# Kernel tuning notes

Hardware: AMD Instinct MI355X
Metric: run time of the kernel (lower is better)

## Reference

```python
import jax, jax.numpy as jnp
import numpy as np

# TT structure: W is [in_features, out_features] = [4096, 4096]
IN_FACTORS = (16, 16, 16)
OUT_FACTORS = (16, 16, 16)
RANKS = (1, 8, 8, 1)
BATCH = 8192
IN_FEATURES = 4096
OUT_FEATURES = 4096
ITER_NUM = 3
L = 1.0
S = -1.0
EPSILON = 1.0


def tt_dense_matmul(cores, mat):
    """Multiply TT-matrix (cores[k]: [r_{k-1}, m_k, n_k, r_k]) by dense mat [prod(n), P].
    Returns [prod(m), P]. Sequential core contractions, never materializes dense W."""
    P = mat.shape[1]
    data = mat.reshape(1, mat.shape[0], P)  # [r=1, N_rem, T]
    M = 1
    for core in cores:
        r0, m, n, r1 = core.shape
        nrem = data.shape[1]
        d4 = data.reshape(r0, n, nrem // n, -1)            # [r0, n_k, N_rem', T]
        data = jnp.einsum('rmns,rnat->satm', core, d4)      # [r1, N_rem', T, m_k]
        data = data.reshape(r1, nrem // n, -1)              # fold m_k into trailing T
        M *= m
    return data.reshape(P, M).T  # [M, P]


def tt_tt_mul(cores_a, cores_b):
    """TT-matrix product: cores of A [M,K] and B [K,N] -> cores of A@B with Kronecker ranks."""
    out = []
    for ca, cb in zip(cores_a, cores_b):
        a0, m, n, a1 = ca.shape
        b0, n2, l, b1 = cb.shape
        c = jnp.einsum('amnb,cnld->acmlbd', ca, cb)
        out.append(c.reshape(a0 * b0, m, l, a1 * b1))
    return out


def setup_inputs() -> dict:
    key = jax.random.key(0)
    ks = jax.random.split(key, 5)
    x = jax.random.normal(ks[0], (BATCH, IN_FEATURES), dtype=jnp.float32)
    # TT cores of weight W [in, out]: core_k shape [r_{k-1}, in_k, out_k, r_k]
    core_std = 0.3  # glorot-like per-core scale
    cores = []
    for k in range(3):
        shp = (RANKS[k], IN_FACTORS[k], OUT_FACTORS[k], RANKS[k + 1])
        cores.append(core_std * jax.random.normal(ks[k + 1], shp, dtype=jnp.float32))
    bias = 0.01 * jnp.ones((OUT_FEATURES,), dtype=jnp.float32)
    return {"x": x, "core0": cores[0], "core1": cores[1], "core2": cores[2], "bias": bias}


def reference(x, core0, core1, core2, bias):
    cores = [core0, core1, core2]
    # weight_t = t3.transpose(weight): swap in/out mode of each core
    cores_t = [c.transpose(0, 2, 1, 3) for c in cores]  # W^T: [out, in]
    x_t = x.T  # [in, B]
    mv = tt_dense_matmul(cores_t, x_t).T  # x @ W, [B, out]
    # norm-gated shrinkage init
    norm_x = jnp.linalg.norm(x)
    x_l = (mv + bias) / L + jnp.where(norm_x > EPSILON, 0.0, S)
    # G = W^T @ W in TT form (ranks grow to 64)
    G = tt_tt_mul(cores_t, cores)
    for _ in range(1, ITER_NUM):
        nrm = jnp.linalg.norm(x_l)
        term = tt_dense_matmul(G, x_l.T).T  # x_l @ (W^T W), [B, out]
        x_l = x_l - term / L + mv / L + bias + jnp.where(nrm > EPSILON, 0.0, S)
    return x_l
```

## Files before the change

### kernel.cpp

```cpp
#include <hip/hip_runtime.h>
#include <stdint.h>

typedef __bf16 bf16;
typedef __bf16 bf16x4 __attribute__((ext_vector_type(4)));
typedef __bf16 bf16x8 __attribute__((ext_vector_type(8)));
typedef float f32x4 __attribute__((ext_vector_type(4)));

#define GLD_LDS16(g, l)                                                        \
  __builtin_amdgcn_global_load_lds(                                            \
      (const __attribute__((address_space(1))) void*)(g),                      \
      (__attribute__((address_space(3))) void*)(l), 16, 0, 0)

#define BAR() asm volatile("s_barrier" ::: "memory")
#define LGKM0() asm volatile("s_waitcnt lgkmcnt(0)" ::: "memory")
#define VMW(n) asm volatile("s_waitcnt vmcnt(" #n ")" ::: "memory")
#define PRIO(x) __builtin_amdgcn_s_setprio(x)

__global__ void k_init(float* s) {
  if (threadIdx.x < 3) s[threadIdx.x] = 0.0f;
}

__global__ void k_cast_ssq(const float* __restrict__ x, bf16* __restrict__ xb,
                           float* __restrict__ ssq, int n4) {
  int tid = blockIdx.x * blockDim.x + threadIdx.x;
  int stride = gridDim.x * blockDim.x;
  const float4* x4 = (const float4*)x;
  bf16x4* xb4 = (bf16x4*)xb;
  float acc = 0.f;
  for (int i = tid; i < n4; i += stride) {
    float4 v = x4[i];
    acc += v.x * v.x + v.y * v.y + v.z * v.z + v.w * v.w;
    bf16x4 b;
    b.x = (bf16)v.x; b.y = (bf16)v.y; b.z = (bf16)v.z; b.w = (bf16)v.w;
    xb4[i] = b;
  }
#pragma unroll
  for (int off = 32; off; off >>= 1) acc += __shfl_down(acc, off);
  __shared__ float red[4];
  if ((threadIdx.x & 63) == 0) red[threadIdx.x >> 6] = acc;
  __syncthreads();
  if (threadIdx.x == 0) atomicAdd(ssq, red[0] + red[1] + red[2] + red[3]);
}

__global__ void k_buildW(const float* __restrict__ c0, const float* __restrict__ c1,
                         const float* __restrict__ c2, bf16* __restrict__ Wt) {
  int t = blockIdx.x * 256 + threadIdx.x;
  int j = t >> 8;
  int i0 = (t >> 4) & 15;
  int i1 = t & 15;
  int j0 = j >> 8, j1 = (j >> 4) & 15, j2 = j & 15;
  float t0[8];
#pragma unroll
  for (int r1 = 0; r1 < 8; ++r1) t0[r1] = c0[(i0 * 16 + j0) * 8 + r1];
  float a[8];
#pragma unroll
  for (int r2 = 0; r2 < 8; ++r2) {
    float s = 0.f;
#pragma unroll
    for (int r1 = 0; r1 < 8; ++r1) s += t0[r1] * c1[((r1 * 16 + i1) * 16 + j1) * 8 + r2];
    a[r2] = s;
  }
  union { bf16 h[16]; bf16x8 v[2]; } u;
#pragma unroll
  for (int i2 = 0; i2 < 16; ++i2) {
    float s = 0.f;
#pragma unroll
    for (int r2 = 0; r2 < 8; ++r2) s += a[r2] * c2[(r2 * 16 + i2) * 16 + j2];
    u.h[i2] = (bf16)s;
  }
  bf16* dst = Wt + (size_t)j * 4096 + i0 * 256 + i1 * 16;
  ((bf16x8*)dst)[0] = u.v[0];
  ((bf16x8*)dst)[1] = u.v[1];
}

template <int MODE>
__global__ __launch_bounds__(512, 2) void k_gemm(
    const bf16* __restrict__ A, const bf16* __restrict__ Bt, int M, int N, int K,
    const float* __restrict__ bias, const bf16* __restrict__ xl0,
    const bf16* __restrict__ xl_prev, float* f32_out, bf16* __restrict__ bf_out,
    const float* __restrict__ ssq_a, const float* __restrict__ ssq_b,
    float* __restrict__ ssq_out) {
  const int nb = gridDim.x * gridDim.y;
  const int lin = blockIdx.y * gridDim.x + blockIdx.x;
  const int sw = (lin & 7) * (nb >> 3) + (lin >> 3);
  const int bx = sw % gridDim.x, by = sw / gridDim.x;
  if constexpr (MODE == 1) {
    if (bx < by) return;
  }

  __shared__ char smem[131072];

  const int t = threadIdx.x;
  const int w = t >> 6, lane = t & 63;
  const int q = lane >> 4, lr = lane & 15;
  const int wm = w & 1, wn = w >> 1;

  float gate = 0.f;
  if constexpr (MODE == 0) {
    gate = (*ssq_a > 1.0f) ? 0.f : -1.f;
  } else if constexpr (MODE == 2 || MODE == 3) {
    float g0 = (*ssq_a > 1.0f) ? 0.f : -1.f;
    float gt = (*ssq_b > 1.0f) ? 0.f : -1.f;
    gate = gt - g0;
  }
  VMW(0);

  const int r0 = t >> 3;
  const int ksrc = (t & 7) ^ (r0 & 7);
  const bf16* srcA = A + (size_t)(by * 256 + r0) * K + ksrc * 8;
  const bf16* srcB = Bt + (size_t)(bx * 256 + r0) * K + ksrc * 8;
  const int wofs = w << 10;

#define STAGE_A(h, kt, b)                                                              \
  do {                                                                                 \
    GLD_LDS16(srcA + (size_t)((h) * 128) * K + (kt) * 64,                              \
              smem + (b) * 65536 + (h) * 16384 + wofs);                                \
    GLD_LDS16(srcA + (size_t)((h) * 128 + 64) * K + (kt) * 64,                         \
              smem + (b) * 65536 + (h) * 16384 + 8192 + wofs);                         \
  } while (0)
#define STAGE_B(h, kt, b)                                                              \
  do {                                                                                 \
    GLD_LDS16(srcB + (size_t)((h) * 128) * K + (kt) * 64,                              \
              smem + (b) * 65536 + 32768 + (h) * 16384 + wofs);                        \
    GLD_LDS16(srcB + (size_t)((h) * 128 + 64) * K + (kt) * 64,                         \
              smem + (b) * 65536 + 32768 + (h) * 16384 + 8192 + wofs);                 \
  } while (0)

  const int aRow = (wm * 64 + lr) * 128;
  const int bRow = (wn * 32 + lr) * 128;
  const int cb0 = ((q ^ (lr & 7)) << 4);
  const int cb1 = (((4 + q) ^ (lr & 7)) << 4);

  f32x4 acc[8][4];
#pragma unroll
  for (int i = 0; i < 8; ++i)
#pragma unroll
    for (int j = 0; j < 4; ++j) acc[i][j] = (f32x4){0.f, 0.f, 0.f, 0.f};

  bf16x8 af[4][2];
  bf16x8 bfr[2][2][2];

#define LDA(ms, b)                                                                     \
  do {                                                                                 \
    const char* s_ = smem + (b) * 65536 + (ms) * 16384 + aRow;                         \
    _Pragma("unroll") for (int mi_ = 0; mi_ < 4; ++mi_) {                              \
      af[mi_][0] = *(const bf16x8*)(s_ + mi_ * 2048 + cb0);                            \
      af[mi_][1] = *(const bf16x8*)(s_ + mi_ * 2048 + cb1);                            \
    }                                                                                  \
  } while (0)
#define LDB(ns, b)                                                                     \
  do {                                                                                 \
    const char* s_ = smem + (b) * 65536 + 32768 + (ns) * 16384 + bRow;                 \
    _Pragma("unroll") for (int ni_ = 0; ni_ < 2; ++ni_) {                              \
      bfr[ns][ni_][0] = *(const bf16x8*)(s_ + ni_ * 2048 + cb0);                       \
      bfr[ns][ni_][1] = *(const bf16x8*)(s_ + ni_ * 2048 + cb1);                       \
    }                                                                                  \
  } while (0)
#define MFMA_Q(ms, ns)                                                                 \
  do {                                                                                 \
    PRIO(1);                                                                           \
    _Pragma("unroll") for (int mi_ = 0; mi_ < 4; ++mi_)                                \
    _Pragma("unroll") for (int ni_ = 0; ni_ < 2; ++ni_)                                \
    _Pragma("unroll") for (int ks_ = 0; ks_ < 2; ++ks_)                                \
        acc[(ms) * 4 + mi_][(ns) * 2 + ni_] =                                          \
            __builtin_amdgcn_mfma_f32_16x16x32_bf16(                                   \
                af[mi_][ks_], bfr[ns][ni_][ks_],                                       \
                acc[(ms) * 4 + mi_][(ns) * 2 + ni_], 0, 0, 0);                         \
    PRIO(0);                                                                           \
  } while (0)

  STAGE_A(0, 0, 0); STAGE_B(0, 0, 0); STAGE_B(1, 0, 0); STAGE_A(1, 0, 0);
  STAGE_A(0, 1, 1); STAGE_B(0, 1, 1); STAGE_B(1, 1, 1);
  VMW(6);
  BAR();

  const int NT = K >> 6;
#pragma unroll 1
  for (int tt = 0; tt < (NT >> 1) - 1; ++tt) {
    const int T = tt << 1;
    LDA(0, 0); LDB(0, 0);
    STAGE_A(1, T + 1, 1);
    BAR(); LGKM0();
    MFMA_Q(0, 0);
    BAR();
    LDB(1, 0);
    STAGE_A(0, T + 2, 0);
    BAR(); LGKM0();
    MFMA_Q(0, 1);
    BAR();
    LDA(1, 0);
    STAGE_B(0, T + 2, 0);
    BAR(); LGKM0();
    MFMA_Q(1, 1);
    BAR();
    STAGE_B(1, T + 2, 0);
    VMW(6);
    BAR();
    MFMA_Q(1, 0);
    BAR();
    LDA(0, 1); LDB(0, 1);
    STAGE_A(1, T + 2, 0);
    BAR(); LGKM0();
    MFMA_Q(0, 0);
    BAR();
    LDB(1, 1);
    STAGE_A(0, T + 3, 1);
    BAR(); LGKM0();
    MFMA_Q(0, 1);
    BAR();
    LDA(1, 1);
    STAGE_B(0, T + 3, 1);
    BAR(); LGKM0();
    MFMA_Q(1, 1);
    BAR();
    STAGE_B(1, T + 3, 1);
    VMW(6);
    BAR();
    MFMA_Q(1, 0);
    BAR();
  }

  LDA(0, 0); LDB(0, 0);
  STAGE_A(1, NT - 1, 1);
  BAR(); LGKM0(); MFMA_Q(0, 0); BAR();
  LDB(1, 0);
  BAR(); LGKM0(); MFMA_Q(0, 1); BAR();
  LDA(1, 0);
  BAR(); LGKM0(); MFMA_Q(1, 1); BAR();
  VMW(0);
  BAR();
  MFMA_Q(1, 0);
  BAR();
  LDA(0, 1); LDB(0, 1);
  BAR(); LGKM0(); MFMA_Q(0, 0); BAR();
  LDB(1, 1);
  BAR(); LGKM0(); MFMA_Q(0, 1); BAR();
  LDA(1, 1);
  BAR(); LGKM0(); MFMA_Q(1, 1); BAR();
  MFMA_Q(1, 0);

  float ssql = 0.f;
#pragma unroll
  for (int mi = 0; mi < 8; ++mi) {
    const int grow = by * 256 + ((mi & 4) ? 128 : 0) + wm * 64 + (mi & 3) * 16 + q * 4;
#pragma unroll
    for (int r = 0; r < 4; ++r) {
      const size_t rowb = (size_t)(grow + r) * N;
#pragma unroll
      for (int ni = 0; ni < 4; ++ni) {
        const int gcol = bx * 256 + ((ni & 2) ? 128 : 0) + wn * 32 + (ni & 1) * 16 + lr;
        const size_t idx = rowb + gcol;
        float v = acc[mi][ni][r];
        if constexpr (MODE == 0) {
          float xl = v + bias[gcol] + gate;
          bf_out[idx] = (bf16)xl;
          ssql += xl * xl;
        } else if constexpr (MODE == 1) {
          bf_out[idx] = (bf16)v;
          if (bx != by) bf_out[(size_t)gcol * N + (grow + r)] = (bf16)v;
        } else if constexpr (MODE == 2) {
          float xl = 2.0f * (float)xl0[idx] - v + gate;
          bf_out[idx] = (bf16)xl;
          ssql += xl * xl;
        } else {
          f32_out[idx] = (float)xl_prev[idx] - v + (float)xl0[idx] + gate;
        }
      }
    }
  }
  if constexpr (MODE == 0 || MODE == 2) {
#pragma unroll
    for (int off = 32; off; off >>= 1) ssql += __shfl_down(ssql, off);
    __syncthreads();
    float* red = (float*)smem;
    if (lane == 0) red[w] = ssql;
    __syncthreads();
    if (t == 0) {
      float s = 0.f;
#pragma unroll
      for (int i = 0; i < 8; ++i) s += red[i];
      atomicAdd(ssq_out, s);
    }
  }
#undef STAGE_A
#undef STAGE_B
#undef LDA
#undef LDB
#undef MFMA_Q
}

extern "C" void kernel_launch(void* const* d_in, const int* in_sizes, int n_in,
                              void* d_out, int out_size, void* d_ws, size_t ws_size,
                              hipStream_t stream) {
  const float* x = (const float*)d_in[0];
  const float* c0 = (const float*)d_in[1];
  const float* c1 = (const float*)d_in[2];
  const float* c2 = (const float*)d_in[3];
  const float* bias = (const float*)d_in[4];
  float* out = (float*)d_out;

  const int B = 8192, F = 4096;
  char* ws = (char*)d_ws;
  float* scal = (float*)ws;
  bf16* xbf = (bf16*)(ws + 256);
  bf16* Wt = (bf16*)(ws + 256 + (size_t)67108864);
  bf16* G = (bf16*)(ws + 256 + (size_t)100663296);
  bf16* xl0 = (bf16*)(ws + 256 + (size_t)134217728);
  bf16* xl1 = xbf;

  k_init<<<1, 64, 0, stream>>>(scal);
  k_cast_ssq<<<1024, 256, 0, stream>>>(x, xbf, &scal[0], B * F / 4);
  k_buildW<<<4096, 256, 0, stream>>>(c0, c1, c2, Wt);

  k_gemm<1><<<dim3(F / 256, F / 256), 512, 0, stream>>>(
      Wt, Wt, F, F, F, nullptr, nullptr, nullptr, nullptr, G, nullptr, nullptr, nullptr);
  dim3 g1(F / 256, B / 256);
  k_gemm<0><<<g1, 512, 0, stream>>>(xbf, Wt, B, F, F, bias, nullptr, nullptr,
                                    nullptr, xl0, &scal[0], nullptr, &scal[1]);
  k_gemm<2><<<g1, 512, 0, stream>>>(xl0, G, B, F, F, nullptr, xl0, nullptr,
                                    nullptr, xl1, &scal[0], &scal[1], &scal[2]);
  k_gemm<3><<<g1, 512, 0, stream>>>(xl1, G, B, F, F, nullptr, xl0, xl1,
                                    out, nullptr, &scal[0], &scal[2], nullptr);
}
```

Baseline: 1.065 ms.

## Merge G and first GEMM into one launch and drop LDS pre-MFMA barriers

Combines the symmetric W^T W GEMM and the x@W GEMM into a single 768-block launch, so the upper-triangle G tiles and the x tiles share one grid and the early-exit G blocks no longer leave the device underfilled. It also restructures the K-loop: the s_barrier plus lgkmcnt(0) wait before each MFMA quarter is removed, and staging is reordered so LDS reads feed MFMAs directly. This relies on compiler-inserted waits for correctness and risks LDS read/write hazards between waves, since fewer barriers separate the global-to-LDS staging from the reads.

Result: no change. 1.055 ms (-0.9%).

```diff
diff --git a/kernel.cpp b/kernel.cpp
--- a/kernel.cpp
+++ b/kernel.cpp
@@ -12,7 +12,6 @@
       (__attribute__((address_space(3))) void*)(l), 16, 0, 0)
 
 #define BAR() asm volatile("s_barrier" ::: "memory")
-#define LGKM0() asm volatile("s_waitcnt lgkmcnt(0)" ::: "memory")
 #define VMW(n) asm volatile("s_waitcnt vmcnt(" #n ")" ::: "memory")
 #define PRIO(x) __builtin_amdgcn_s_setprio(x)
 
@@ -73,44 +72,6 @@
   ((bf16x8*)dst)[1] = u.v[1];
 }
 
-template <int MODE>
-__global__ __launch_bounds__(512, 2) void k_gemm(
-    const bf16* __restrict__ A, const bf16* __restrict__ Bt, int M, int N, int K,
-    const float* __restrict__ bias, const bf16* __restrict__ xl0,
-    const bf16* __restrict__ xl_prev, float* f32_out, bf16* __restrict__ bf_out,
-    const float* __restrict__ ssq_a, const float* __restrict__ ssq_b,
-    float* __restrict__ ssq_out) {
-  const int nb = gridDim.x * gridDim.y;
-  const int lin = blockIdx.y * gridDim.x + blockIdx.x;
-  const int sw = (lin & 7) * (nb >> 3) + (lin >> 3);
-  const int bx = sw % gridDim.x, by = sw / gridDim.x;
-  if constexpr (MODE == 1) {
-    if (bx < by) return;
-  }
-
-  __shared__ char smem[131072];
-
-  const int t = threadIdx.x;
-  const int w = t >> 6, lane = t & 63;
-  const int q = lane >> 4, lr = lane & 15;
-  const int wm = w & 1, wn = w >> 1;
-
-  float gate = 0.f;
-  if constexpr (MODE == 0) {
-    gate = (*ssq_a > 1.0f) ? 0.f : -1.f;
-  } else if constexpr (MODE == 2 || MODE == 3) {
-    float g0 = (*ssq_a > 1.0f) ? 0.f : -1.f;
-    float gt = (*ssq_b > 1.0f) ? 0.f : -1.f;
-    gate = gt - g0;
-  }
-  VMW(0);
-
-  const int r0 = t >> 3;
-  const int ksrc = (t & 7) ^ (r0 & 7);
-  const bf16* srcA = A + (size_t)(by * 256 + r0) * K + ksrc * 8;
-  const bf16* srcB = Bt + (size_t)(bx * 256 + r0) * K + ksrc * 8;
-  const int wofs = w << 10;
-
 #define STAGE_A(h, kt, b)                                                              \
   do {                                                                                 \
     GLD_LDS16(srcA + (size_t)((h) * 128) * K + (kt) * 64,                              \
@@ -125,21 +86,6 @@
     GLD_LDS16(srcB + (size_t)((h) * 128 + 64) * K + (kt) * 64,                         \
               smem + (b) * 65536 + 32768 + (h) * 16384 + 8192 + wofs);                 \
   } while (0)
-
-  const int aRow = (wm * 64 + lr) * 128;
-  const int bRow = (wn * 32 + lr) * 128;
-  const int cb0 = ((q ^ (lr & 7)) << 4);
-  const int cb1 = (((4 + q) ^ (lr & 7)) << 4);
-
-  f32x4 acc[8][4];
-#pragma unroll
-  for (int i = 0; i < 8; ++i)
-#pragma unroll
-    for (int j = 0; j < 4; ++j) acc[i][j] = (f32x4){0.f, 0.f, 0.f, 0.f};
-
-  bf16x8 af[4][2];
-  bf16x8 bfr[2][2][2];
-
 #define LDA(ms, b)                                                                     \
   do {                                                                                 \
     const char* s_ = smem + (b) * 65536 + (ms) * 16384 + aRow;                         \
@@ -169,6 +115,34 @@
     PRIO(0);                                                                           \
   } while (0)
 
+__device__ __forceinline__ void run_core(const bf16* __restrict__ Ag,
+                                         const bf16* __restrict__ Bg, const int K,
+                                         const int bx, const int by, char* smem,
+                                         f32x4 (&acc)[8][4]) {
+  const int t = threadIdx.x;
+  const int w = t >> 6, lane = t & 63;
+  const int q = lane >> 4, lr = lane & 15;
+  const int wm = w & 1, wn = w >> 1;
+
+  const int r0 = t >> 3;
+  const int ksrc = (t & 7) ^ (r0 & 7);
+  const bf16* srcA = Ag + (size_t)(by * 256 + r0) * K + ksrc * 8;
+  const bf16* srcB = Bg + (size_t)(bx * 256 + r0) * K + ksrc * 8;
+  const int wofs = w << 10;
+
+  const int aRow = (wm * 64 + lr) * 128;
+  const int bRow = (wn * 32 + lr) * 128;
+  const int cb0 = ((q ^ (lr & 7)) << 4);
+  const int cb1 = (((4 + q) ^ (lr & 7)) << 4);
+
+#pragma unroll
+  for (int i = 0; i < 8; ++i)
+#pragma unroll
+    for (int j = 0; j < 4; ++j) acc[i][j] = (f32x4){0.f, 0.f, 0.f, 0.f};
+
+  bf16x8 af[4][2];
+  bf16x8 bfr[2][2][2];
+
   STAGE_A(0, 0, 0); STAGE_B(0, 0, 0); STAGE_B(1, 0, 0); STAGE_A(1, 0, 0);
   STAGE_A(0, 1, 1); STAGE_B(0, 1, 1); STAGE_B(1, 1, 1);
   VMW(6);
@@ -178,67 +152,88 @@
 #pragma unroll 1
   for (int tt = 0; tt < (NT >> 1) - 1; ++tt) {
     const int T = tt << 1;
-    LDA(0, 0); LDB(0, 0);
     STAGE_A(1, T + 1, 1);
-    BAR(); LGKM0();
+    LDB(0, 0); LDA(0, 0);
     MFMA_Q(0, 0);
     BAR();
+    STAGE_A(0, T + 2, 0);
     LDB(1, 0);
-    STAGE_A(0, T + 2, 0);
-    BAR(); LGKM0();
     MFMA_Q(0, 1);
     BAR();
+    STAGE_B(0, T + 2, 0);
     LDA(1, 0);
-    STAGE_B(0, T + 2, 0);
-    BAR(); LGKM0();
     MFMA_Q(1, 1);
     BAR();
     STAGE_B(1, T + 2, 0);
+    MFMA_Q(1, 0);
     VMW(6);
     BAR();
+    STAGE_A(1, T + 2, 0);
+    LDB(0, 1); LDA(0, 1);
+    MFMA_Q(0, 0);
+    BAR();
+    STAGE_A(0, T + 3, 1);
+    LDB(1, 1);
+    MFMA_Q(0, 1);
+    BAR();
+    STAGE_B(0, T + 3, 1);
+    LDA(1, 1);
+    MFMA_Q(1, 1);
+    BAR();
+    STAGE_B(1, T + 3, 1);
     MFMA_Q(1, 0);
-    BAR();
-    LDA(0, 1); LDB(0, 1);
-    STAGE_A(1, T + 2, 0);
-    BAR(); LGKM0();
-    MFMA_Q(0, 0);
-    BAR();
-    LDB(1, 1);
-    STAGE_A(0, T + 3, 1);
-    BAR(); LGKM0();
-    MFMA_Q(0, 1);
-    BAR();
-    LDA(1, 1);
-    STAGE_B(0, T + 3, 1);
-    BAR(); LGKM0();
-    MFMA_Q(1, 1);
-    BAR();
-    STAGE_B(1, T + 3, 1);
     VMW(6);
     BAR();
-    MFMA_Q(1, 0);
-    BAR();
-  }
-
-  LDA(0, 0); LDB(0, 0);
+  }
+
   STAGE_A(1, NT - 1, 1);
-  BAR(); LGKM0(); MFMA_Q(0, 0); BAR();
+  LDB(0, 0); LDA(0, 0);
+  MFMA_Q(0, 0); BAR();
   LDB(1, 0);
-  BAR(); LGKM0(); MFMA_Q(0, 1); BAR();
+  MFMA_Q(0, 1); BAR();
   LDA(1, 0);
-  BAR(); LGKM0(); MFMA_Q(1, 1); BAR();
+  MFMA_Q(1, 1); BAR();
+  MFMA_Q(1, 0);
   VMW(0);
   BAR();
+  LDB(0, 1); LDA(0, 1);
+  MFMA_Q(0, 0); BAR();
+  LDB(1, 1);
+  MFMA_Q(0, 1); BAR();
+  LDA(1, 1);
+  MFMA_Q(1, 1); BAR();
   MFMA_Q(1, 0);
-  BAR();
-  LDA(0, 1); LDB(0, 1);
-  BAR(); LGKM0(); MFMA_Q(0, 0); BAR();
-  LDB(1, 1);
-  BAR(); LGKM0(); MFMA_Q(0, 1); BAR();
-  LDA(1, 1);
-  BAR(); LGKM0(); MFMA_Q(1, 1); BAR();
-  MFMA_Q(1, 0);
-
+}
+
+__global__ __launch_bounds__(512, 2) void k_gemm01(
+    const bf16* __restrict__ xbf, const bf16* __restrict__ Wt,
+    const float* __restrict__ bias, bf16* __restrict__ Gout,
+    bf16* __restrict__ xl0, const float* __restrict__ ssq_x,
+    float* __restrict__ ssq_out) {
+  const int lin = blockIdx.x;
+  const int sw = (lin & 7) * 96 + (lin >> 3);
+  int bx, by;
+  bool isG;
+  if (sw < 256) {
+    isG = true; bx = sw & 15; by = sw >> 4;
+    if (bx < by) return;
+  } else {
+    isG = false; int r = sw - 256; bx = r & 15; by = r >> 4;
+  }
+  __shared__ char smem[131072];
+
+  float gate = 0.f;
+  if (!isG) gate = (*ssq_x > 1.0f) ? 0.f : -1.f;
+  VMW(0);
+
+  f32x4 acc[8][4];
+  run_core(isG ? Wt : xbf, Wt, 4096, bx, by, smem, acc);
+
+  const int t = threadIdx.x;
+  const int w = t >> 6, lane = t & 63;
+  const int q = lane >> 4, lr = lane & 15;
+  const int wm = w & 1, wn = w >> 1;
+  const int N = 4096;
   float ssql = 0.f;
 #pragma unroll
   for (int mi = 0; mi < 8; ++mi) {
@@ -251,14 +246,72 @@
         const int gcol = bx * 256 + ((ni & 2) ? 128 : 0) + wn * 32 + (ni & 1) * 16 + lr;
         const size_t idx = rowb + gcol;
         float v = acc[mi][ni][r];
-        if constexpr (MODE == 0) {
+        if (isG) {
+          Gout[idx] = (bf16)v;
+          if (bx != by) Gout[(size_t)gcol * N + (grow + r)] = (bf16)v;
+        } else {
           float xl = v + bias[gcol] + gate;
-          bf_out[idx] = (bf16)xl;
+          xl0[idx] = (bf16)xl;
           ssql += xl * xl;
-        } else if constexpr (MODE == 1) {
-          bf_out[idx] = (bf16)v;
-          if (bx != by) bf_out[(size_t)gcol * N + (grow + r)] = (bf16)v;
-        } else if constexpr (MODE == 2) {
+        }
+      }
+    }
+  }
+  if (!isG) {
+#pragma unroll
+    for (int off = 32; off; off >>= 1) ssql += __shfl_down(ssql, off);
+    __syncthreads();
+    float* red = (float*)smem;
+    if (lane == 0) red[w] = ssql;
+    __syncthreads();
+    if (t == 0) {
+      float s = 0.f;
+#pragma unroll
+      for (int i = 0; i < 8; ++i) s += red[i];
+      atomicAdd(ssq_out, s);
+    }
+  }
+}
+
+template <int MODE>
+__global__ __launch_bounds__(512, 2) void k_gemm23(
+    const bf16* __restrict__ A, const bf16* __restrict__ Gt,
+    const bf16* __restrict__ xl0, const bf16* __restrict__ xl_prev,
+    float* __restrict__ f32_out, bf16* __restrict__ bf_out,
+    const float* __restrict__ ssq_a, const float* __restrict__ ssq_b,
+    float* __restrict__ ssq_out) {
+  const int nb = gridDim.x * gridDim.y;
+  const int lin = blockIdx.y * gridDim.x + blockIdx.x;
+  const int sw = (lin & 7) * (nb >> 3) + (lin >> 3);
+  const int bx = sw % gridDim.x, by = sw / gridDim.x;
+  __shared__ char smem[131072];
+
+  const float g0 = (*ssq_a > 1.0f) ? 0.f : -1.f;
+  const float gt = (*ssq_b > 1.0f) ? 0.f : -1.f;
+  const float gate = gt - g0;
+  VMW(0);
+
+  f32x4 acc[8][4];
+  run_core(A, Gt, 4096, bx, by, smem, acc);
+
+  const int t = threadIdx.x;
+  const int w = t >> 6, lane = t & 63;
+  const int q = lane >> 4, lr = lane & 15;
+  const int wm = w & 1, wn = w >> 1;
+  const int N = 4096;
+  float ssql = 0.f;
+#pragma unroll
+  for (int mi = 0; mi < 8; ++mi) {
+    const int grow = by * 256 + ((mi & 4) ? 128 : 0) + wm * 64 + (mi & 3) * 16 + q * 4;
+#pragma unroll
+    for (int r = 0; r < 4; ++r) {
+      const size_t rowb = (size_t)(grow + r) * N;
+#pragma unroll
+      for (int ni = 0; ni < 4; ++ni) {
+        const int gcol = bx * 256 + ((ni & 2) ? 128 : 0) + wn * 32 + (ni & 1) * 16 + lr;
+        const size_t idx = rowb + gcol;
+        float v = acc[mi][ni][r];
+        if constexpr (MODE == 2) {
           float xl = 2.0f * (float)xl0[idx] - v + gate;
           bf_out[idx] = (bf16)xl;
           ssql += xl * xl;
@@ -268,7 +321,7 @@
       }
     }
   }
-  if constexpr (MODE == 0 || MODE == 2) {
+  if constexpr (MODE == 2) {
 #pragma unroll
     for (int off = 32; off; off >>= 1) ssql += __shfl_down(ssql, off);
     __syncthreads();
@@ -282,11 +335,6 @@
       atomicAdd(ssq_out, s);
     }
   }
-#undef STAGE_A
-#undef STAGE_B
-#undef LDA
-#undef LDB
-#undef MFMA_Q
 }
 
 extern "C" void kernel_launch(void* const* d_in, const int* in_sizes, int n_in,
@@ -312,13 +360,10 @@
   k_cast_ssq<<<1024, 256, 0, stream>>>(x, xbf, &scal[0], B * F / 4);
   k_buildW<<<4096, 256, 0, stream>>>(c0, c1, c2, Wt);
 
-  k_gemm<1><<<dim3(F / 256, F / 256), 512, 0, stream>>>(
-      Wt, Wt, F, F, F, nullptr, nullptr, nullptr, nullptr, G, nullptr, nullptr, nullptr);
+  k_gemm01<<<768, 512, 0, stream>>>(xbf, Wt, bias, G, xl0, &scal[0], &scal[1]);
   dim3 g1(F / 256, B / 256);
-  k_gemm<0><<<g1, 512, 0, stream>>>(xbf, Wt, B, F, F, bias, nullptr, nullptr,
-                                    nullptr, xl0, &scal[0], nullptr, &scal[1]);
-  k_gemm<2><<<g1, 512, 0, stream>>>(xl0, G, B, F, F, nullptr, xl0, nullptr,
-                                    nullptr, xl1, &scal[0], &scal[1], &scal[2]);
-  k_gemm<3><<<g1, 512, 0, stream>>>(xl1, G, B, F, F, nullptr, xl0, xl1,
-                                    out, nullptr, &scal[0], &scal[2], nullptr);
-}
+  k_gemm23<2><<<g1, 512, 0, stream>>>(xl0, G, xl0, nullptr, nullptr, xl1,
+                                      &scal[0], &scal[1], &scal[2]);
+  k_gemm23<3><<<g1, 512, 0, stream>>>(xl1, G, xl0, xl1, out, nullptr,
+                                      &scal[0], &scal[2], nullptr);
+}
```

## Build G from TT core Gram products and re-pipeline GEMM LDS loads

Applied to the files above, without the earlier changes.

Replaces the dense W^T W GEMM (4096^3) with a TT-structured construction: per-core Gram tensors are computed in a small kernel, then G is assembled by contracting the rank-64 cores in a dedicated kernel. Separately, the main GEMM loop is rescheduled so LDS fragment loads for the next quarter overlap with the current MFMA quarter, using double-buffered B fragments and dropping the explicit lgkmcnt waits and some barriers. This removes a large GEMM from the pipeline but adds a scalar-FP32 G build kernel and relies on compiler-inserted waits for LDS reads being correct.

Result: faster. 983.0 us (-7.7%).

```diff
diff --git a/kernel.cpp b/kernel.cpp
--- a/kernel.cpp
+++ b/kernel.cpp
@@ -12,7 +12,6 @@
       (__attribute__((address_space(3))) void*)(l), 16, 0, 0)
 
 #define BAR() asm volatile("s_barrier" ::: "memory")
-#define LGKM0() asm volatile("s_waitcnt lgkmcnt(0)" ::: "memory")
 #define VMW(n) asm volatile("s_waitcnt vmcnt(" #n ")" ::: "memory")
 #define PRIO(x) __builtin_amdgcn_s_setprio(x)
 
@@ -73,43 +72,112 @@
   ((bf16x8*)dst)[1] = u.v[1];
 }
 
-template <int MODE>
-__global__ __launch_bounds__(512, 2) void k_gemm(
-    const bf16* __restrict__ A, const bf16* __restrict__ Bt, int M, int N, int K,
-    const float* __restrict__ bias, const bf16* __restrict__ xl0,
-    const bf16* __restrict__ xl_prev, float* f32_out, bf16* __restrict__ bf_out,
-    const float* __restrict__ ssq_a, const float* __restrict__ ssq_b,
-    float* __restrict__ ssq_out) {
-  const int nb = gridDim.x * gridDim.y;
-  const int lin = blockIdx.y * gridDim.x + blockIdx.x;
-  const int sw = (lin & 7) * (nb >> 3) + (lin >> 3);
-  const int bx = sw % gridDim.x, by = sw / gridDim.x;
-  if constexpr (MODE == 1) {
-    if (bx < by) return;
-  }
-
-  __shared__ char smem[131072];
-
+__global__ __launch_bounds__(256) void k_gcores(const float* __restrict__ c0,
+                                                const float* __restrict__ c1,
+                                                const float* __restrict__ c2,
+                                                float* __restrict__ g0,
+                                                float* __restrict__ g1,
+                                                float* __restrict__ g2) {
+  int tid = blockIdx.x * 256 + threadIdx.x;
+  if (tid < 16384) {
+    int jj = tid >> 6, p1 = tid & 63;
+    int j0 = jj >> 4, j0p = jj & 15, r1 = p1 >> 3, r1p = p1 & 7;
+    float s = 0.f;
+#pragma unroll
+    for (int i0 = 0; i0 < 16; ++i0)
+      s += c0[(i0 * 16 + j0) * 8 + r1] * c0[(i0 * 16 + j0p) * 8 + r1p];
+    g0[tid] = s;
+  } else if (tid < 32768) {
+    int k = tid - 16384;
+    int p2 = k >> 8, jj = k & 255;
+    int r2 = p2 >> 3, r2p = p2 & 7, j2 = jj >> 4, j2p = jj & 15;
+    float s = 0.f;
+#pragma unroll
+    for (int i2 = 0; i2 < 16; ++i2)
+      s += c2[(r2 * 16 + i2) * 16 + j2] * c2[(r2p * 16 + i2) * 16 + j2p];
+    g2[k] = s;
+  } else {
+    int k = tid - 32768;
+    int p2 = k & 63, rest = k >> 6;
+    int j1p = rest & 15, j1 = (rest >> 4) & 15, p1 = rest >> 8;
+    int r1 = p1 >> 3, r1p = p1 & 7, r2 = p2 >> 3, r2p = p2 & 7;
+    float s = 0.f;
+#pragma unroll
+    for (int i1 = 0; i1 < 16; ++i1)
+      s += c1[((r1 * 16 + i1) * 16 + j1) * 8 + r2] *
+           c1[((r1p * 16 + i1) * 16 + j1p) * 8 + r2p];
+    g1[k] = s;
+  }
+}
+
+__global__ __launch_bounds__(256) void k_buildG(const float* __restrict__ g0,
+                                                const float* __restrict__ g1,
+                                                const float* __restrict__ g2,
+                                                bf16* __restrict__ G) {
+  __shared__ float s_g2[16384];
+  __shared__ float s_g1[4096];
+  __shared__ float s_g0t[16384];
   const int t = threadIdx.x;
-  const int w = t >> 6, lane = t & 63;
-  const int q = lane >> 4, lr = lane & 15;
-  const int wm = w & 1, wn = w >> 1;
-
-  float gate = 0.f;
-  if constexpr (MODE == 0) {
-    gate = (*ssq_a > 1.0f) ? 0.f : -1.f;
-  } else if constexpr (MODE == 2 || MODE == 3) {
-    float g0 = (*ssq_a > 1.0f) ? 0.f : -1.f;
-    float gt = (*ssq_b > 1.0f) ? 0.f : -1.f;
-    gate = gt - g0;
-  }
-  VMW(0);
-
-  const int r0 = t >> 3;
-  const int ksrc = (t & 7) ^ (r0 & 7);
-  const bf16* srcA = A + (size_t)(by * 256 + r0) * K + ksrc * 8;
-  const bf16* srcB = Bt + (size_t)(bx * 256 + r0) * K + ksrc * 8;
-  const int wofs = w << 10;
+  const int j1 = blockIdx.x >> 4, j1p = blockIdx.x & 15;
+  const int jj1 = j1 * 16 + j1p;
+
+  const float4* g2f4 = (const float4*)g2;
+  float4* sg2f4 = (float4*)s_g2;
+  for (int k = t; k < 4096; k += 256) sg2f4[k] = g2f4[k];
+  const float4* g1f4 = (const float4*)g1;
+  float4* sg1f4 = (float4*)s_g1;
+  for (int k = t; k < 1024; k += 256) {
+    int p1 = k >> 4, q = k & 15;
+    sg1f4[k] = g1f4[(p1 * 256 + jj1) * 16 + q];
+  }
+#pragma unroll
+  for (int q = 0; q < 16; ++q) {
+    float4 v = ((const float4*)g0)[t * 16 + q];
+    s_g0t[(q * 4 + 0) * 256 + t] = v.x;
+    s_g0t[(q * 4 + 1) * 256 + t] = v.y;
+    s_g0t[(q * 4 + 2) * 256 + t] = v.z;
+    s_g0t[(q * 4 + 3) * 256 + t] = v.w;
+  }
+  __syncthreads();
+
+  float m[64];
+#pragma unroll
+  for (int i = 0; i < 64; ++i) m[i] = 0.f;
+#pragma unroll 4
+  for (int p1 = 0; p1 < 64; ++p1) {
+    float av = s_g0t[p1 * 256 + t];
+#pragma unroll
+    for (int q = 0; q < 16; ++q) {
+      float4 v = ((const float4*)s_g1)[p1 * 16 + q];
+      m[q * 4 + 0] += av * v.x; m[q * 4 + 1] += av * v.y;
+      m[q * 4 + 2] += av * v.z; m[q * 4 + 3] += av * v.w;
+    }
+  }
+
+  const int j0 = t >> 4, j0p = t & 15;
+  bf16* gb = G + (size_t)(j0 * 256 + j1 * 16) * 4096 + (j0p * 256 + j1p * 16);
+  for (int j2 = 0; j2 < 16; ++j2) {
+    float o[16];
+#pragma unroll
+    for (int i = 0; i < 16; ++i) o[i] = 0.f;
+#pragma unroll
+    for (int p2 = 0; p2 < 64; ++p2) {
+      const float4* r = (const float4*)s_g2 + p2 * 64 + j2 * 4;
+#pragma unroll
+      for (int q = 0; q < 4; ++q) {
+        float4 v = r[q];
+        o[q * 4 + 0] += m[p2] * v.x; o[q * 4 + 1] += m[p2] * v.y;
+        o[q * 4 + 2] += m[p2] * v.z; o[q * 4 + 3] += m[p2] * v.w;
+      }
+    }
+    union { bf16 h[16]; bf16x8 v[2]; } u;
+#pragma unroll
+    for (int i = 0; i < 16; ++i) u.h[i] = (bf16)o[i];
+    bf16* d = gb + (size_t)j2 * 4096;
+    ((bf16x8*)d)[0] = u.v[0];
+    ((bf16x8*)d)[1] = u.v[1];
+  }
+}
 
 #define STAGE_A(h, kt, b)                                                              \
   do {                                                                                 \
@@ -125,21 +193,6 @@
     GLD_LDS16(srcB + (size_t)((h) * 128 + 64) * K + (kt) * 64,                         \
               smem + (b) * 65536 + 32768 + (h) * 16384 + 8192 + wofs);                 \
   } while (0)
-
-  const int aRow = (wm * 64 + lr) * 128;
-  const int bRow = (wn * 32 + lr) * 128;
-  const int cb0 = ((q ^ (lr & 7)) << 4);
-  const int cb1 = (((4 + q) ^ (lr & 7)) << 4);
-
-  f32x4 acc[8][4];
-#pragma unroll
-  for (int i = 0; i < 8; ++i)
-#pragma unroll
-    for (int j = 0; j < 4; ++j) acc[i][j] = (f32x4){0.f, 0.f, 0.f, 0.f};
-
-  bf16x8 af[4][2];
-  bf16x8 bfr[2][2][2];
-
 #define LDA(ms, b)                                                                     \
   do {                                                                                 \
     const char* s_ = smem + (b) * 65536 + (ms) * 16384 + aRow;                         \
@@ -148,15 +201,15 @@
       af[mi_][1] = *(const bf16x8*)(s_ + mi_ * 2048 + cb1);                            \
     }                                                                                  \
   } while (0)
-#define LDB(ns, b)                                                                     \
+#define LDBX(ns, b, DST)                                                               \
   do {                                                                                 \
     const char* s_ = smem + (b) * 65536 + 32768 + (ns) * 16384 + bRow;                 \
     _Pragma("unroll") for (int ni_ = 0; ni_ < 2; ++ni_) {                              \
-      bfr[ns][ni_][0] = *(const bf16x8*)(s_ + ni_ * 2048 + cb0);                       \
-      bfr[ns][ni_][1] = *(const bf16x8*)(s_ + ni_ * 2048 + cb1);                       \
+      DST[ni_][0] = *(const bf16x8*)(s_ + ni_ * 2048 + cb0);                           \
+      DST[ni_][1] = *(const bf16x8*)(s_ + ni_ * 2048 + cb1);                           \
     }                                                                                  \
   } while (0)
-#define MFMA_Q(ms, ns)                                                                 \
+#define MQ(ms, ns, BSRC)                                                               \
   do {                                                                                 \
     PRIO(1);                                                                           \
     _Pragma("unroll") for (int mi_ = 0; mi_ < 4; ++mi_)                                \
@@ -164,81 +217,138 @@
     _Pragma("unroll") for (int ks_ = 0; ks_ < 2; ++ks_)                                \
         acc[(ms) * 4 + mi_][(ns) * 2 + ni_] =                                          \
             __builtin_amdgcn_mfma_f32_16x16x32_bf16(                                   \
-                af[mi_][ks_], bfr[ns][ni_][ks_],                                       \
+                af[mi_][ks_], BSRC[ni_][ks_],                                          \
                 acc[(ms) * 4 + mi_][(ns) * 2 + ni_], 0, 0, 0);                         \
     PRIO(0);                                                                           \
   } while (0)
+
+__device__ __forceinline__ void run_core(const bf16* __restrict__ Ag,
+                                         const bf16* __restrict__ Bg, const int K,
+                                         const int bx, const int by, char* smem,
+                                         f32x4 (&acc)[8][4]) {
+  const int t = threadIdx.x;
+  const int w = t >> 6, lane = t & 63;
+  const int q = lane >> 4, lr = lane & 15;
+  const int wm = w & 1, wn = w >> 1;
+
+  const int r0 = t >> 3;
+  const int ksrc = (t & 7) ^ (r0 & 7);
+  const bf16* srcA = Ag + (size_t)(by * 256 + r0) * K + ksrc * 8;
+  const bf16* srcB = Bg + (size_t)(bx * 256 + r0) * K + ksrc * 8;
+  const int wofs = w << 10;
+
+  const int aRow = (wm * 64 + lr) * 128;
+  const int bRow = (wn * 32 + lr) * 128;
+  const int cb0 = ((q ^ (lr & 7)) << 4);
+  const int cb1 = (((4 + q) ^ (lr & 7)) << 4);
+
+#pragma unroll
+  for (int i = 0; i < 8; ++i)
+#pragma unroll
+    for (int j = 0; j < 4; ++j) acc[i][j] = (f32x4){0.f, 0.f, 0.f, 0.f};
+
+  bf16x8 af[4][2];
+  bf16x8 bfr1[2][2];
+  bf16x8 bfr0A[2][2];
+  bf16x8 bfr0B[2][2];
 
   STAGE_A(0, 0, 0); STAGE_B(0, 0, 0); STAGE_B(1, 0, 0); STAGE_A(1, 0, 0);
   STAGE_A(0, 1, 1); STAGE_B(0, 1, 1); STAGE_B(1, 1, 1);
   VMW(6);
   BAR();
+  LDBX(0, 0, bfr0A);
 
   const int NT = K >> 6;
 #pragma unroll 1
   for (int tt = 0; tt < (NT >> 1) - 1; ++tt) {
     const int T = tt << 1;
-    LDA(0, 0); LDB(0, 0);
     STAGE_A(1, T + 1, 1);
-    BAR(); LGKM0();
-    MFMA_Q(0, 0);
-    BAR();
-    LDB(1, 0);
+    LDA(0, 0);
+    MQ(0, 0, bfr0A);
+    BAR();
     STAGE_A(0, T + 2, 0);
-    BAR(); LGKM0();
-    MFMA_Q(0, 1);
-    BAR();
+    LDBX(1, 0, bfr1);
+    MQ(0, 1, bfr1);
+    BAR();
+    STAGE_B(0, T + 2, 0);
     LDA(1, 0);
-    STAGE_B(0, T + 2, 0);
-    BAR(); LGKM0();
-    MFMA_Q(1, 1);
+    MQ(1, 1, bfr1);
+    VMW(4);
     BAR();
     STAGE_B(1, T + 2, 0);
-    VMW(6);
-    BAR();
-    MFMA_Q(1, 0);
-    BAR();
-    LDA(0, 1); LDB(0, 1);
+    LDBX(0, 1, bfr0B);
+    MQ(1, 0, bfr0A);
+    BAR();
     STAGE_A(1, T + 2, 0);
-    BAR(); LGKM0();
-    MFMA_Q(0, 0);
-    BAR();
-    LDB(1, 1);
+    LDA(0, 1);
+    MQ(0, 0, bfr0B);
+    BAR();
     STAGE_A(0, T + 3, 1);
-    BAR(); LGKM0();
-    MFMA_Q(0, 1);
-    BAR();
+    LDBX(1, 1, bfr1);
+    MQ(0, 1, bfr1);
+    BAR();
+    STAGE_B(0, T + 3, 1);
     LDA(1, 1);
-    STAGE_B(0, T + 3, 1);
-    BAR(); LGKM0();
-    MFMA_Q(1, 1);
+    MQ(1, 1, bfr1);
+    VMW(4);
     BAR();
     STAGE_B(1, T + 3, 1);
-    VMW(6);
-    BAR();
-    MFMA_Q(1, 0);
-    BAR();
-  }
-
-  LDA(0, 0); LDB(0, 0);
+    LDBX(0, 0, bfr0A);
+    MQ(1, 0, bfr0B);
+    BAR();
+  }
+
   STAGE_A(1, NT - 1, 1);
-  BAR(); LGKM0(); MFMA_Q(0, 0); BAR();
-  LDB(1, 0);
-  BAR(); LGKM0(); MFMA_Q(0, 1); BAR();
+  LDA(0, 0);
+  MQ(0, 0, bfr0A); BAR();
+  LDBX(1, 0, bfr1);
+  MQ(0, 1, bfr1); BAR();
   LDA(1, 0);
-  BAR(); LGKM0(); MFMA_Q(1, 1); BAR();
+  MQ(1, 1, bfr1);
   VMW(0);
   BAR();
-  MFMA_Q(1, 0);
+  LDBX(0, 1, bfr0B);
+  MQ(1, 0, bfr0A);
   BAR();
-  LDA(0, 1); LDB(0, 1);
-  BAR(); LGKM0(); MFMA_Q(0, 0); BAR();
-  LDB(1, 1);
-  BAR(); LGKM0(); MFMA_Q(0, 1); BAR();
+  LDA(0, 1);
+  MQ(0, 0, bfr0B); BAR();
+  LDBX(1, 1, bfr1);
+  MQ(0, 1, bfr1); BAR();
   LDA(1, 1);
-  BAR(); LGKM0(); MFMA_Q(1, 1); BAR();
-  MFMA_Q(1, 0);
-
+  MQ(1, 1, bfr1); BAR();
+  MQ(1, 0, bfr0B);
+}
+
+template <int MODE>
+__global__ __launch_bounds__(512, 2) void k_gemm(
+    const bf16* __restrict__ A, const bf16* __restrict__ Bt, int M, int N, int K,
+    const float* __restrict__ bias, const bf16* __restrict__ xl0,
+    const bf16* __restrict__ xl_prev, float* f32_out, bf16* __restrict__ bf_out,
+    const float* __restrict__ ssq_a, const float* __restrict__ ssq_b,
+    float* __restrict__ ssq_out) {
+  const int nb = gridDim.x * gridDim.y;
+  const int lin = blockIdx.y * gridDim.x + blockIdx.x;
+  const int sw = (lin & 7) * (nb >> 3) + (lin >> 3);
+  const int bx = sw % gridDim.x, by = sw / gridDim.x;
+  __shared__ char smem[131072];
+
+  float gate = 0.f;
+  if constexpr (MODE == 0) {
+    gate = (*ssq_a > 1.0f) ? 0.f : -1.f;
+  } else {
+    float g0v = (*ssq_a > 1.0f) ? 0.f : -1.f;
+    float gtv = (*ssq_b > 1.0f) ? 0.f : -1.f;
+    gate = gtv - g0v;
+  }
+  VMW(0);
+
+  f32x4 acc[8][4];
+  run_core(A, Bt, K, bx, by, smem, acc);
+
+  const int t = threadIdx.x;
+  const int w = t >> 6, lane = t & 63;
+  const int q = lane >> 4, lr = lane & 15;
+  const int wm = w & 1, wn = w >> 1;
   float ssql = 0.f;
 #pragma unroll
   for (int mi = 0; mi < 8; ++mi) {
@@ -255,9 +365,6 @@
           float xl = v + bias[gcol] + gate;
           bf_out[idx] = (bf16)xl;
           ssql += xl * xl;
-        } else if constexpr (MODE == 1) {
-          bf_out[idx] = (bf16)v;
-          if (bx != by) bf_out[(size_t)gcol * N + (grow + r)] = (bf16)v;
         } else if constexpr (MODE == 2) {
           float xl = 2.0f * (float)xl0[idx] - v + gate;
           bf_out[idx] = (bf16)xl;
@@ -282,11 +389,6 @@
       atomicAdd(ssq_out, s);
     }
   }
-#undef STAGE_A
-#undef STAGE_B
-#undef LDA
-#undef LDB
-#undef MFMA_Q
 }
 
 extern "C" void kernel_launch(void* const* d_in, const int* in_sizes, int n_in,
@@ -307,18 +409,22 @@
   bf16* G = (bf16*)(ws + 256 + (size_t)100663296);
   bf16* xl0 = (bf16*)(ws + 256 + (size_t)134217728);
   bf16* xl1 = xbf;
+  float* g0 = (float*)xl0;
+  float* g2 = g0 + 16384;
+  float* g1 = g2 + 16384;
 
   k_init<<<1, 64, 0, stream>>>(scal);
   k_cast_ssq<<<1024, 256, 0, stream>>>(x, xbf, &scal[0], B * F / 4);
   k_buildW<<<4096, 256, 0, stream>>>(c0, c1, c2, Wt);
 
-  k_gemm<1><<<dim3(F / 256, F / 256), 512, 0, stream>>>(
-      Wt, Wt, F, F, F, nullptr, nullptr, nullptr, nullptr, G, nullptr, nullptr, nullptr);
-  dim3 g1(F / 256, B / 256);
-  k_gemm<0><<<g1, 512, 0, stream>>>(xbf, Wt, B, F, F, bias, nullptr, nullptr,
-                                    nullptr, xl0, &scal[0], nullptr, &scal[1]);
-  k_gemm<2><<<g1, 512, 0, stream>>>(xl0, G, B, F, F, nullptr, xl0, nullptr,
-                                    nullptr, xl1, &scal[0], &scal[1], &scal[2]);
-  k_gemm<3><<<g1, 512, 0, stream>>>(xl1, G, B, F, F, nullptr, xl0, xl1,
-                                    out, nullptr, &scal[0], &scal[2], nullptr);
-}
+  k_gcores<<<4224, 256, 0, stream>>>(c0, c1, c2, g0, g1, g2);
+  k_buildG<<<256, 256, 0, stream>>>(g0, g1, g2, G);
+
+  dim3 g1d(F / 256, B / 256);
+  k_gemm<0><<<g1d, 512, 0, stream>>>(xbf, Wt, B, F, F, bias, nullptr, nullptr,
+                                     nullptr, xl0, &scal[0], nullptr, &scal[1]);
+  k_gemm<2><<<g1d, 512, 0, stream>>>(xl0, G, B, F, F, nullptr, xl0, nullptr,
+                                     nullptr, xl1, &scal[0], &scal[1], &scal[2]);
+  k_gemm<3><<<g1d, 512, 0, stream>>>(xl1, G, B, F, F, nullptr, xl0, xl1,
+                                     out, nullptr, &scal[0], &scal[2], nullptr);
+}
```
